# Optimization experiments

Hardware: AMD Instinct MI355X
Metric: run time of the kernel (lower is better)

## Reference

```python
import jax, jax.numpy as jnp
import numpy as np

N_EL = 4            # allowed elements (H, C, N, O)
N_EXPERTS = N_EL * N_EL
F_ATOM = 176        # per-atom symmetry feature dim
F_PAIR = 32         # pair feature dim (2*F_ATOM + F_PAIR == 384 == nodes[0])


def _init_linear(key, fin, fout, n):
    # torch nn.Linear default init: U(-1/sqrt(fin), 1/sqrt(fin))
    bound = 1.0 / np.sqrt(fin)
    kw, kb = jax.random.split(key)
    W = jax.random.uniform(kw, (n, fin, fout), minval=-bound, maxval=bound, dtype=jnp.float32)
    b = jax.random.uniform(kb, (n, fout), minval=-bound, maxval=bound, dtype=jnp.float32)
    return W, b


def setup_inputs() -> dict:
    key = jax.random.key(0)
    ks = jax.random.split(key, 8)
    B, A, C = 128, 128, 256
    elements = jax.random.randint(ks[0], (B, A), 0, N_EL)
    connectivity = jax.random.randint(ks[1], (B, C, 2), 0, A)
    sym_features = jax.random.normal(ks[2], (B, A, F_ATOM), dtype=jnp.float32)
    pair_features = jax.random.normal(ks[3], (B, C, F_PAIR), dtype=jnp.float32)
    W1, b1 = _init_linear(ks[4], 384, 128, N_EXPERTS)
    W2, b2 = _init_linear(ks[5], 128, 96, N_EXPERTS)
    W3, b3 = _init_linear(ks[6], 96, 2, N_EXPERTS)
    return dict(elements=elements, connectivity=connectivity,
                sym_features=sym_features, pair_features=pair_features,
                W1=W1, b1=b1, W2=W2, b2=b2, W3=W3, b3=b3)


def _pair_moe(elements, connectivity, sym_features, pair_features, W1, b1, W2, b2, W3, b3):
    B, C, _ = connectivity.shape
    A = sym_features.shape[1]
    out_dim = W3.shape[-1]

    # mirror: mask padded pairs (connectivity[...,0] == -1) before offsetting
    mask = (connectivity[..., 0] != -1).reshape(-1)              # [B*C]
    conn_f = (connectivity + (jnp.arange(B) * A)[:, None, None]).reshape(-1, 2)
    idx0 = jnp.where(mask, conn_f[:, 0], 0)
    idx1 = jnp.where(mask, conn_f[:, 1], 0)

    feat_f = sym_features.reshape(-1, sym_features.shape[-1])    # [B*A, F]
    el_f = elements.reshape(-1)                                  # [B*A]

    m = mask[:, None].astype(sym_features.dtype)
    fa = feat_f[idx0] * m                                        # [B*C, F] (zeros where padded)
    fb = feat_f[idx1] * m
    e0 = jnp.where(mask, el_f[idx0], -1)
    e1 = jnp.where(mask, el_f[idx1], -1)
    nn_index = e0 * N_EL + e1                                    # -5 for padded pairs -> no expert

    x = jnp.concatenate([fa, fb, pair_features.reshape(-1, pair_features.shape[-1])], axis=1)

    y = jnp.zeros((x.shape[0], out_dim), dtype=x.dtype)
    for i in range(N_EXPERTS):  # fixed small expert set (structural loop)
        h = jax.nn.celu(x @ W1[i] + b1[i])
        h = jax.nn.celu(h @ W2[i] + b2[i])
        o = h @ W3[i] + b3[i]
        y = jnp.where((nn_index == i)[:, None], o, y)
    return y.reshape(B, C, out_dim)


def reference(elements, connectivity, sym_features, pair_features, W1, b1, W2, b2, W3, b3):
    # Original returns (elements, connectivity, y); only y is computed output.
    return _pair_moe(elements, connectivity, sym_features, pair_features, W1, b1, W2, b2, W3, b3)
```

## Files before the change

kernel.cpp:

```cpp
#include <hip/hip_runtime.h>
#include <math.h>

typedef __attribute__((ext_vector_type(8))) short short8;
typedef __attribute__((ext_vector_type(4))) float f32x4;

namespace {
constexpr int NEL   = 4;
constexpr int NEXP  = 16;
constexpr int Bb    = 128;
constexpr int Aa    = 128;
constexpr int Cc    = 256;
constexpr int FATOM = 176;
constexpr int FPAIR = 32;
constexpr int FIN   = 384;
constexpr int HH1   = 128;
constexpr int HH2   = 96;
constexpr int NP    = Bb * Cc;
constexpr int BUCKET_CAP = 4096;

constexpr int WS_COUNTS = 0;
constexpr int WS_BUCKET = 64;
constexpr int WS_BF     = 65600;
constexpr int SYM_N   = Bb * Aa * FATOM;
constexpr int PAIR_N  = Bb * Cc * FPAIR;

constexpr int W2_OFF = 12 * HH1 * 32;
constexpr int WPK_E  = W2_OFF + 4 * HH2 * 32;

constexpr int CVT_BLOCKS = (SYM_N / 4 + PAIR_N / 4) / 256;
constexpr int W1_BLOCKS  = 768;
constexpr int W2_BLOCKS  = 192;
constexpr int IDX_BLOCKS = NP / 256;
constexpr int W1_BASE  = CVT_BLOCKS;
constexpr int W2_BASE  = W1_BASE + W1_BLOCKS;
constexpr int IDX_BASE = W2_BASE + W2_BLOCKS;
constexpr int PREP_GRID = IDX_BASE + IDX_BLOCKS;
}

__device__ inline float bf2f(short s) {
    unsigned u = ((unsigned)(unsigned short)s) << 16;
    return __builtin_bit_cast(float, u);
}
__device__ inline short f2bf(float f) {
    unsigned u = __builtin_bit_cast(unsigned, f);
    unsigned r = (u + 0x7FFFu + ((u >> 16) & 1u)) >> 16;
    return (short)r;
}
__device__ inline float celu1(float v) {
    return v > 0.f ? v : (__expf(v) - 1.0f);
}

__global__ __launch_bounds__(256) void k_prep(
    const float* __restrict__ sym, const float* __restrict__ pairf,
    short* __restrict__ symb, short* __restrict__ pairfb,
    const float* __restrict__ W1, const float* __restrict__ W2,
    short* __restrict__ wpk,
    const int* __restrict__ conn, const int* __restrict__ elements,
    int* __restrict__ counts, int* __restrict__ bucket,
    float* __restrict__ out)
{
    __shared__ float T[32][33];
    __shared__ int sh_cnt[NEXP], sh_base[NEXP];

    int bid = blockIdx.x;
    int t = threadIdx.x;

    if (bid < CVT_BLOCKS) {
        int i = bid * 256 + t;
        constexpr int NS4 = SYM_N / 4;
        const float4* src; short* dst; int j;
        if (i < NS4) { src = (const float4*)sym;   dst = symb;   j = i; }
        else         { src = (const float4*)pairf; dst = pairfb; j = i - NS4; }
        float4 v = src[j];
        short4 o;
        o.x = f2bf(v.x); o.y = f2bf(v.y); o.z = f2bf(v.z); o.w = f2bf(v.w);
        *(short4*)(dst + 4 * (size_t)j) = o;
    } else if (bid < IDX_BASE) {
        const float* src; short* dst; int K, N, k0, n0;
        if (bid < W2_BASE) {
            int b1i = bid - W1_BASE;
            int e = b1i / 48, tl = b1i % 48;
            K = FIN; N = HH1; k0 = (tl % 12) * 32; n0 = (tl / 12) * 32;
            src = W1 + (size_t)e * K * N;
            dst = wpk + (size_t)e * WPK_E;
        } else {
            int b2i = bid - W2_BASE;
            int e = b2i / 12, tl = b2i % 12;
            K = HH1; N = HH2; k0 = (tl % 4) * 32; n0 = (tl / 4) * 32;
            src = W2 + (size_t)e * K * N;
            dst = wpk + (size_t)e * WPK_E + W2_OFF;
        }
        int tx = t & 31, ty = t >> 5;
        int ks = k0 >> 5;
#pragma unroll
        for (int j = 0; j < 4; ++j) {
            int r = ty + 8 * j;
            T[r][tx] = src[(size_t)(k0 + r) * N + n0 + tx];
        }
        __syncthreads();
#pragma unroll
        for (int j = 0; j < 4; ++j) {
            int n = n0 + ty + 8 * j;
            dst[(size_t)(ks * N + n) * 32 + tx] = f2bf(T[tx][ty + 8 * j]);
        }
    } else {
        int p = (bid - IDX_BASE) * 256 + t;
        if (t < NEXP) sh_cnt[t] = 0;
        __syncthreads();
        int e = -1, r = 0;
        {
            int c0 = conn[2 * p], c1 = conn[2 * p + 1];
            if (c0 != -1) {
                int b = p / Cc;
                int i0 = b * Aa + c0; if (i0 < 0) i0 += Bb * Aa;
                int i1 = b * Aa + c1; if (i1 < 0) i1 += Bb * Aa;
                e = elements[i0] * NEL + elements[i1];
            }
            if (e < 0 || e >= NEXP) {
                out[2 * p] = 0.f; out[2 * p + 1] = 0.f;
                e = -1;
            } else {
                r = atomicAdd(&sh_cnt[e], 1);
            }
        }
        __syncthreads();
        if (t < NEXP) sh_base[t] = (sh_cnt[t] > 0) ? atomicAdd(&counts[t], sh_cnt[t]) : 0;
        __syncthreads();
        if (e >= 0) {
            int pos = sh_base[e] + r;
            if (pos < BUCKET_CAP) bucket[e * BUCKET_CAP + pos] = p;
        }
    }
}

__global__ __launch_bounds__(512, 2) void k_moe(
    const int* __restrict__ counts, const int* __restrict__ bucket,
    const int* __restrict__ conn,
    const short* __restrict__ symb, const short* __restrict__ pairfb,
    const short* __restrict__ wpk,
    const float* __restrict__ b1, const float* __restrict__ b2,
    const float* __restrict__ W3, const float* __restrict__ b3,
    float* __restrict__ out)
{
    __shared__ short Wlds[WPK_E];
    __shared__ short H1s[8][16 * HH1];

    int e     = blockIdx.x & 15;
    int shard = blockIdx.x >> 4;
    int cnt = counts[e];
    if (cnt > BUCKET_CAP) cnt = BUCKET_CAP;

    int t = threadIdx.x;
    int w = t >> 6;
    int lane = t & 63;
    int lr = lane & 15, lg = (lane >> 4) & 3;

    const short* wsrc = wpk + (size_t)e * WPK_E;
    {
        short8 v[15];
#pragma unroll
        for (int r = 0; r < 15; ++r) v[r] = *(const short8*)(wsrc + r * 4096 + t * 8);
#pragma unroll
        for (int r = 0; r < 15; ++r) *(short8*)&Wlds[r * 4096 + t * 8] = v[r];
    }

    float b1v[8];
#pragma unroll
    for (int j = 0; j < 8; ++j) b1v[j] = b1[e * HH1 + j * 16 + lr];
    float2 b3v = ((const float2*)b3)[e];

    __syncthreads();

    int nt = (cnt + 15) >> 4;
    const int* bucket_e = bucket + e * BUCKET_CAP;
    short* h1w = &H1s[w][0];

    for (int tile = shard * 8 + w; tile < nt; tile += 128) {
        int ii = tile * 16 + lr;
        int p = bucket_e[ii < cnt ? ii : cnt - 1];
        int2 c = ((const int2*)conn)[p];
        int bb = (p >> 8) << 7;
        const short* fa = symb + (size_t)(bb + c.x) * FATOM;
        const short* fb = symb + (size_t)(bb + c.y) * FATOM;
        const short* pf = pairfb + (size_t)p * FPAIR;

        short8 a[12];
        a[0]  = *(const short8*)(fa + 8 * lg);
        a[1]  = *(const short8*)(fa + 32 + 8 * lg);
        a[2]  = *(const short8*)(fa + 64 + 8 * lg);
        a[3]  = *(const short8*)(fa + 96 + 8 * lg);
        a[4]  = *(const short8*)(fa + 128 + 8 * lg);
        a[5]  = *(const short8*)((lg < 2 ? fa + 160 : fb - 16) + 8 * lg);
        a[6]  = *(const short8*)(fb + 16 + 8 * lg);
        a[7]  = *(const short8*)(fb + 48 + 8 * lg);
        a[8]  = *(const short8*)(fb + 80 + 8 * lg);
        a[9]  = *(const short8*)(fb + 112 + 8 * lg);
        a[10] = *(const short8*)(fb + 144 + 8 * lg);
        a[11] = *(const short8*)(pf + 8 * lg);

        f32x4 acc[8];
#pragma unroll
        for (int j = 0; j < 8; ++j) acc[j] = (f32x4){b1v[j], b1v[j], b1v[j], b1v[j]};
#pragma unroll
        for (int ks = 0; ks < 12; ++ks) {
#pragma unroll
            for (int j = 0; j < 8; ++j) {
                short8 bw = *(const short8*)&Wlds[(ks * HH1 + j * 16 + lr) * 32 + 8 * lg];
                acc[j] = __builtin_amdgcn_mfma_f32_16x16x32_bf16(a[ks], bw, acc[j], 0, 0, 0);
            }
        }

#pragma unroll
        for (int j = 0; j < 8; ++j)
#pragma unroll
            for (int r2 = 0; r2 < 4; ++r2) {
                int m = 4 * lg + r2;
                int n = 16 * j + lr;
                h1w[m * HH1 + (((n >> 3) ^ (m & 7)) << 3) + (n & 7)] = f2bf(celu1(acc[j][r2]));
            }
        asm volatile("s_waitcnt lgkmcnt(0)" ::: "memory");
        __builtin_amdgcn_sched_barrier(0);

        int mx = lr & 7;
        short8 bh[4];
#pragma unroll
        for (int q = 0; q < 4; ++q)
            bh[q] = *(const short8*)&h1w[lr * HH1 + (((q * 4 + lg) ^ mx) << 3)];

        float s0 = 0.f, s1 = 0.f;
#pragma unroll
        for (int t6 = 0; t6 < 6; ++t6) {
            int n2b = 16 * t6 + 4 * lg;
            float4 bb4 = *(const float4*)&b2[e * HH2 + n2b];
            f32x4 a2;
            a2[0] = bb4.x; a2[1] = bb4.y; a2[2] = bb4.z; a2[3] = bb4.w;
#pragma unroll
            for (int q = 0; q < 4; ++q) {
                short8 aw = *(const short8*)&Wlds[W2_OFF + (q * HH2 + 16 * t6 + lr) * 32 + 8 * lg];
                a2 = __builtin_amdgcn_mfma_f32_16x16x32_bf16(aw, bh[q], a2, 0, 0, 0);
            }
            float4 w3a = *(const float4*)&W3[(size_t)(e * HH2 + n2b) * 2];
            float4 w3b = *(const float4*)&W3[(size_t)(e * HH2 + n2b) * 2 + 4];
            float h0 = celu1(a2[0]), h1 = celu1(a2[1]), h2 = celu1(a2[2]), h3 = celu1(a2[3]);
            s0 = fmaf(h0, w3a.x, fmaf(h1, w3a.z, fmaf(h2, w3b.x, fmaf(h3, w3b.z, s0))));
            s1 = fmaf(h0, w3a.y, fmaf(h1, w3a.w, fmaf(h2, w3b.y, fmaf(h3, w3b.w, s1))));
        }
        s0 += __shfl_xor(s0, 16); s0 += __shfl_xor(s0, 32);
        s1 += __shfl_xor(s1, 16); s1 += __shfl_xor(s1, 32);
        if (((lane >> 4) & 3) == 0 && ii < cnt) {
            float2 o2; o2.x = s0 + b3v.x; o2.y = s1 + b3v.y;
            *(float2*)(out + 2 * (size_t)bucket_e[ii]) = o2;
        }
    }
}

extern "C" void kernel_launch(void* const* d_in, const int* in_sizes, int n_in,
                              void* d_out, int out_size, void* d_ws, size_t ws_size,
                              hipStream_t stream)
{
    const int*   elements = (const int*)d_in[0];
    const int*   conn     = (const int*)d_in[1];
    const float* sym      = (const float*)d_in[2];
    const float* pairf    = (const float*)d_in[3];
    const float* W1       = (const float*)d_in[4];
    const float* b1       = (const float*)d_in[5];
    const float* W2       = (const float*)d_in[6];
    const float* b2       = (const float*)d_in[7];
    const float* W3       = (const float*)d_in[8];
    const float* b3       = (const float*)d_in[9];
    float* out = (float*)d_out;

    int* wsi    = (int*)d_ws;
    int* counts = wsi + WS_COUNTS;
    int* bucket = wsi + WS_BUCKET;

    short* bfb    = (short*)(wsi + WS_BF);
    short* symb   = bfb;
    short* pairfb = bfb + SYM_N;
    short* wpk    = bfb + SYM_N + PAIR_N;

    hipMemsetAsync((void*)counts, 0, NEXP * sizeof(int), stream);

    k_prep<<<PREP_GRID, 256, 0, stream>>>(sym, pairf, symb, pairfb,
                                          W1, W2, wpk,
                                          conn, elements, counts, bucket, out);
    k_moe<<<256, 512, 0, stream>>>(counts, bucket, conn, symb, pairfb, wpk,
                                   b1, b2, W3, b3, out);
}
```

Before: 35.74 us.

## Fuse bf16 conversion of features and weights into the MoE kernel

Drops the separate prep pass that converted symmetry features, pair features and W1/W2 to bf16 workspace buffers. The MoE kernel now reads fp32 features directly and converts them in registers, and each block packs its expert's weights from fp32 into LDS itself. This removes a large write-then-read round trip through global memory. In exchange, gathered feature loads are twice as wide, and each of the 256 blocks redundantly converts its expert weights using strided, uncoalesced fp32 loads.

Result: slower. 38.49 us (+7.7%).

```diff
diff --git a/kernel.cpp b/kernel.cpp
--- a/kernel.cpp
+++ b/kernel.cpp
@@ -20,27 +20,11 @@
 
 constexpr int WS_COUNTS = 0;
 constexpr int WS_BUCKET = 64;
-constexpr int WS_BF     = 65600;
-constexpr int SYM_N   = Bb * Aa * FATOM;
-constexpr int PAIR_N  = Bb * Cc * FPAIR;
 
 constexpr int W2_OFF = 12 * HH1 * 32;
 constexpr int WPK_E  = W2_OFF + 4 * HH2 * 32;
-
-constexpr int CVT_BLOCKS = (SYM_N / 4 + PAIR_N / 4) / 256;
-constexpr int W1_BLOCKS  = 768;
-constexpr int W2_BLOCKS  = 192;
-constexpr int IDX_BLOCKS = NP / 256;
-constexpr int W1_BASE  = CVT_BLOCKS;
-constexpr int W2_BASE  = W1_BASE + W1_BLOCKS;
-constexpr int IDX_BASE = W2_BASE + W2_BLOCKS;
-constexpr int PREP_GRID = IDX_BASE + IDX_BLOCKS;
-}
-
-__device__ inline float bf2f(short s) {
-    unsigned u = ((unsigned)(unsigned short)s) << 16;
-    return __builtin_bit_cast(float, u);
-}
+}
+
 __device__ inline short f2bf(float f) {
     unsigned u = __builtin_bit_cast(unsigned, f);
     unsigned r = (u + 0x7FFFu + ((u >> 16) & 1u)) >> 16;
@@ -49,95 +33,55 @@
 __device__ inline float celu1(float v) {
     return v > 0.f ? v : (__expf(v) - 1.0f);
 }
-
-__global__ __launch_bounds__(256) void k_prep(
-    const float* __restrict__ sym, const float* __restrict__ pairf,
-    short* __restrict__ symb, short* __restrict__ pairfb,
-    const float* __restrict__ W1, const float* __restrict__ W2,
-    short* __restrict__ wpk,
+__device__ inline short8 cvt8(const float* p) {
+    float4 lo = *(const float4*)p;
+    float4 hi = *(const float4*)(p + 4);
+    short8 r;
+    r[0] = f2bf(lo.x); r[1] = f2bf(lo.y); r[2] = f2bf(lo.z); r[3] = f2bf(lo.w);
+    r[4] = f2bf(hi.x); r[5] = f2bf(hi.y); r[6] = f2bf(hi.z); r[7] = f2bf(hi.w);
+    return r;
+}
+
+__global__ __launch_bounds__(256) void k_idx(
     const int* __restrict__ conn, const int* __restrict__ elements,
     int* __restrict__ counts, int* __restrict__ bucket,
     float* __restrict__ out)
 {
-    __shared__ float T[32][33];
     __shared__ int sh_cnt[NEXP], sh_base[NEXP];
-
-    int bid = blockIdx.x;
     int t = threadIdx.x;
-
-    if (bid < CVT_BLOCKS) {
-        int i = bid * 256 + t;
-        constexpr int NS4 = SYM_N / 4;
-        const float4* src; short* dst; int j;
-        if (i < NS4) { src = (const float4*)sym;   dst = symb;   j = i; }
-        else         { src = (const float4*)pairf; dst = pairfb; j = i - NS4; }
-        float4 v = src[j];
-        short4 o;
-        o.x = f2bf(v.x); o.y = f2bf(v.y); o.z = f2bf(v.z); o.w = f2bf(v.w);
-        *(short4*)(dst + 4 * (size_t)j) = o;
-    } else if (bid < IDX_BASE) {
-        const float* src; short* dst; int K, N, k0, n0;
-        if (bid < W2_BASE) {
-            int b1i = bid - W1_BASE;
-            int e = b1i / 48, tl = b1i % 48;
-            K = FIN; N = HH1; k0 = (tl % 12) * 32; n0 = (tl / 12) * 32;
-            src = W1 + (size_t)e * K * N;
-            dst = wpk + (size_t)e * WPK_E;
+    int p = blockIdx.x * 256 + t;
+    if (t < NEXP) sh_cnt[t] = 0;
+    __syncthreads();
+    int e = -1, r = 0;
+    {
+        int c0 = conn[2 * p], c1 = conn[2 * p + 1];
+        if (c0 != -1) {
+            int b = p / Cc;
+            int i0 = b * Aa + c0; if (i0 < 0) i0 += Bb * Aa;
+            int i1 = b * Aa + c1; if (i1 < 0) i1 += Bb * Aa;
+            e = elements[i0] * NEL + elements[i1];
+        }
+        if (e < 0 || e >= NEXP) {
+            out[2 * p] = 0.f; out[2 * p + 1] = 0.f;
+            e = -1;
         } else {
-            int b2i = bid - W2_BASE;
-            int e = b2i / 12, tl = b2i % 12;
-            K = HH1; N = HH2; k0 = (tl % 4) * 32; n0 = (tl / 4) * 32;
-            src = W2 + (size_t)e * K * N;
-            dst = wpk + (size_t)e * WPK_E + W2_OFF;
-        }
-        int tx = t & 31, ty = t >> 5;
-        int ks = k0 >> 5;
-#pragma unroll
-        for (int j = 0; j < 4; ++j) {
-            int r = ty + 8 * j;
-            T[r][tx] = src[(size_t)(k0 + r) * N + n0 + tx];
-        }
-        __syncthreads();
-#pragma unroll
-        for (int j = 0; j < 4; ++j) {
-            int n = n0 + ty + 8 * j;
-            dst[(size_t)(ks * N + n) * 32 + tx] = f2bf(T[tx][ty + 8 * j]);
-        }
-    } else {
-        int p = (bid - IDX_BASE) * 256 + t;
-        if (t < NEXP) sh_cnt[t] = 0;
-        __syncthreads();
-        int e = -1, r = 0;
-        {
-            int c0 = conn[2 * p], c1 = conn[2 * p + 1];
-            if (c0 != -1) {
-                int b = p / Cc;
-                int i0 = b * Aa + c0; if (i0 < 0) i0 += Bb * Aa;
-                int i1 = b * Aa + c1; if (i1 < 0) i1 += Bb * Aa;
-                e = elements[i0] * NEL + elements[i1];
-            }
-            if (e < 0 || e >= NEXP) {
-                out[2 * p] = 0.f; out[2 * p + 1] = 0.f;
-                e = -1;
-            } else {
-                r = atomicAdd(&sh_cnt[e], 1);
-            }
-        }
-        __syncthreads();
-        if (t < NEXP) sh_base[t] = (sh_cnt[t] > 0) ? atomicAdd(&counts[t], sh_cnt[t]) : 0;
-        __syncthreads();
-        if (e >= 0) {
-            int pos = sh_base[e] + r;
-            if (pos < BUCKET_CAP) bucket[e * BUCKET_CAP + pos] = p;
-        }
+            r = atomicAdd(&sh_cnt[e], 1);
+        }
+    }
+    __syncthreads();
+    if (t < NEXP) sh_base[t] = (sh_cnt[t] > 0) ? atomicAdd(&counts[t], sh_cnt[t]) : 0;
+    __syncthreads();
+    if (e >= 0) {
+        int pos = sh_base[e] + r;
+        if (pos < BUCKET_CAP) bucket[e * BUCKET_CAP + pos] = p;
     }
 }
 
 __global__ __launch_bounds__(512, 2) void k_moe(
     const int* __restrict__ counts, const int* __restrict__ bucket,
     const int* __restrict__ conn,
-    const short* __restrict__ symb, const short* __restrict__ pairfb,
-    const short* __restrict__ wpk,
+    const float* __restrict__ sym, const float* __restrict__ pairf,
+    const float* __restrict__ W1, const float* __restrict__ W2,
     const float* __restrict__ b1, const float* __restrict__ b2,
     const float* __restrict__ W3, const float* __restrict__ b3,
     float* __restrict__ out)
@@ -155,13 +99,34 @@
     int lane = t & 63;
     int lr = lane & 15, lg = (lane >> 4) & 3;
 
-    const short* wsrc = wpk + (size_t)e * WPK_E;
     {
-        short8 v[15];
-#pragma unroll
-        for (int r = 0; r < 15; ++r) v[r] = *(const short8*)(wsrc + r * 4096 + t * 8);
-#pragma unroll
-        for (int r = 0; r < 15; ++r) *(short8*)&Wlds[r * 4096 + t * 8] = v[r];
+        const float* W1e = W1 + (size_t)e * FIN * HH1;
+#pragma unroll
+        for (int rr = 0; rr < 3; ++rr) {
+            int s = t + 512 * rr;
+            int ks = s >> 7, n = s & 127;
+            const float* src = W1e + (size_t)(ks * 32) * HH1 + n;
+#pragma unroll
+            for (int q = 0; q < 4; ++q) {
+                short8 v;
+#pragma unroll
+                for (int j = 0; j < 8; ++j)
+                    v[j] = f2bf(src[(size_t)(q * 8 + j) * HH1]);
+                *(short8*)&Wlds[(ks * HH1 + n) * 32 + 8 * q] = v;
+            }
+        }
+        if (t < 384) {
+            int q4 = t / 96, n2 = t % 96;
+            const float* src = W2 + (size_t)e * HH1 * HH2 + (size_t)(q4 * 32) * HH2 + n2;
+#pragma unroll
+            for (int q = 0; q < 4; ++q) {
+                short8 v;
+#pragma unroll
+                for (int j = 0; j < 8; ++j)
+                    v[j] = f2bf(src[(size_t)(q * 8 + j) * HH2]);
+                *(short8*)&Wlds[W2_OFF + (q4 * HH2 + n2) * 32 + 8 * q] = v;
+            }
+        }
     }
 
     float b1v[8];
@@ -180,23 +145,23 @@
         int p = bucket_e[ii < cnt ? ii : cnt - 1];
         int2 c = ((const int2*)conn)[p];
         int bb = (p >> 8) << 7;
-        const short* fa = symb + (size_t)(bb + c.x) * FATOM;
-        const short* fb = symb + (size_t)(bb + c.y) * FATOM;
-        const short* pf = pairfb + (size_t)p * FPAIR;
+        const float* fa = sym + (size_t)(bb + c.x) * FATOM;
+        const float* fb = sym + (size_t)(bb + c.y) * FATOM;
+        const float* pf = pairf + (size_t)p * FPAIR;
 
         short8 a[12];
-        a[0]  = *(const short8*)(fa + 8 * lg);
-        a[1]  = *(const short8*)(fa + 32 + 8 * lg);
-        a[2]  = *(const short8*)(fa + 64 + 8 * lg);
-        a[3]  = *(const short8*)(fa + 96 + 8 * lg);
-        a[4]  = *(const short8*)(fa + 128 + 8 * lg);
-        a[5]  = *(const short8*)((lg < 2 ? fa + 160 : fb - 16) + 8 * lg);
-        a[6]  = *(const short8*)(fb + 16 + 8 * lg);
-        a[7]  = *(const short8*)(fb + 48 + 8 * lg);
-        a[8]  = *(const short8*)(fb + 80 + 8 * lg);
-        a[9]  = *(const short8*)(fb + 112 + 8 * lg);
-        a[10] = *(const short8*)(fb + 144 + 8 * lg);
-        a[11] = *(const short8*)(pf + 8 * lg);
+        a[0]  = cvt8(fa + 8 * lg);
+        a[1]  = cvt8(fa + 32 + 8 * lg);
+        a[2]  = cvt8(fa + 64 + 8 * lg);
+        a[3]  = cvt8(fa + 96 + 8 * lg);
+        a[4]  = cvt8(fa + 128 + 8 * lg);
+        a[5]  = cvt8((lg < 2 ? fa + 160 : fb - 16) + 8 * lg);
+        a[6]  = cvt8(fb + 16 + 8 * lg);
+        a[7]  = cvt8(fb + 48 + 8 * lg);
+        a[8]  = cvt8(fb + 80 + 8 * lg);
+        a[9]  = cvt8(fb + 112 + 8 * lg);
+        a[10] = cvt8(fb + 144 + 8 * lg);
+        a[11] = cvt8(pf + 8 * lg);
 
         f32x4 acc[8];
 #pragma unroll
@@ -274,16 +239,9 @@
     int* counts = wsi + WS_COUNTS;
     int* bucket = wsi + WS_BUCKET;
 
-    short* bfb    = (short*)(wsi + WS_BF);
-    short* symb   = bfb;
-    short* pairfb = bfb + SYM_N;
-    short* wpk    = bfb + SYM_N + PAIR_N;
-
     hipMemsetAsync((void*)counts, 0, NEXP * sizeof(int), stream);
 
-    k_prep<<<PREP_GRID, 256, 0, stream>>>(sym, pairf, symb, pairfb,
-                                          W1, W2, wpk,
-                                          conn, elements, counts, bucket, out);
-    k_moe<<<256, 512, 0, stream>>>(counts, bucket, conn, symb, pairfb, wpk,
-                                   b1, b2, W3, b3, out);
-}
+    k_idx<<<NP / 256, 256, 0, stream>>>(conn, elements, counts, bucket, out);
+    k_moe<<<256, 512, 0, stream>>>(counts, bucket, conn, sym, pairf,
+                                   W1, W2, b1, b2, W3, b3, out);
+}
```
